# Optimization experiments

Hardware: AMD Instinct MI355X
Metric: run time of the kernel (lower is better)

Reference implementation:

```python
import jax, jax.numpy as jnp
import numpy as np

N_NODES = 50000


def sage_conv(x, src, dst, Wl, bl, Wr, n_nodes):
    # PyG SAGEConv (aggr='mean', root_weight=True, bias on lin_l):
    #   out = lin_l(mean_{j in N(i)} x_j) + lin_r(x_i)
    msg = x[src]  # [E, d] gather
    s = jax.ops.segment_sum(msg, dst, num_segments=n_nodes)  # [N, d]
    cnt = jax.ops.segment_sum(jnp.ones((src.shape[0], 1), x.dtype), dst,
                              num_segments=n_nodes)  # [N, 1]
    agg = s / jnp.maximum(cnt, 1.0)
    return agg @ Wl.T + bl + x @ Wr.T


def setup_inputs() -> dict:
    key = jax.random.key(0)
    ks = jax.random.split(key, 8)
    in_c, hid_c, out_c = 256, 256, 2
    x = jax.random.normal(ks[0], (N_NODES, in_c), dtype=jnp.float32)
    edge_index = jax.random.randint(ks[1], (2, 800000), 0, N_NODES, dtype=jnp.int64)
    def lin(k, fan_out, fan_in):
        bound = 1.0 / np.sqrt(fan_in)
        return jax.random.uniform(k, (fan_out, fan_in), jnp.float32, -bound, bound)
    return {
        "x": x,
        "edge_index": edge_index,
        "W1l": lin(ks[2], hid_c, in_c),
        "b1": jnp.zeros((hid_c,), jnp.float32),
        "W1r": lin(ks[3], hid_c, in_c),
        "W2l": lin(ks[4], out_c, hid_c),
        "b2": jnp.zeros((out_c,), jnp.float32),
        "W2r": lin(ks[5], out_c, hid_c),
    }


def reference(x, edge_index, W1l, b1, W1r, W2l, b2, W2r):
    src, dst = edge_index[0], edge_index[1]
    h = sage_conv(x, src, dst, W1l, b1, W1r, N_NODES)
    h = jax.nn.relu(h)
    # dropout is identity in eval mode (training=False)
    out = sage_conv(h, src, dst, W2l, b2, W2r, N_NODES)
    return jax.nn.log_softmax(out, axis=1)
```

## Files before the change

### kernel.cpp

```cpp
#include <hip/hip_runtime.h>
#include <math.h>

#define DIM 256
#define GBM 128
#define GBN 128
#define GBK 64
#define LDS_K 72
#define SCHUNK 1024

typedef short bf16x8 __attribute__((ext_vector_type(8)));
typedef float f32x4 __attribute__((ext_vector_type(4)));

__device__ __forceinline__ ushort f2bf(float f) {
  uint u = __float_as_uint(f);
  u += 0x7fffu + ((u >> 16) & 1u);
  return (ushort)(u >> 16);
}
__device__ __forceinline__ float bf2f(uint bits) {
  return __uint_as_float(bits << 16);
}

__global__ __launch_bounds__(256) void convert_x(
    const float4* __restrict__ x4, ushort* __restrict__ xb, int n4) {
  int i = blockIdx.x * blockDim.x + threadIdx.x;
  const int stride = gridDim.x * blockDim.x;
  for (; i < n4; i += stride) {
    const float4 v = x4[i];
    ushort4 o;
    o.x = f2bf(v.x); o.y = f2bf(v.y); o.z = f2bf(v.z); o.w = f2bf(v.w);
    *(ushort4*)&xb[i * 4] = o;
  }
}

__global__ __launch_bounds__(256) void wcat_kernel(
    const float* __restrict__ Wl, const float* __restrict__ Wr,
    const float* __restrict__ W2l, const float* __restrict__ W2r,
    ushort* __restrict__ Wb, ushort* __restrict__ W2b) {
  const int idx = blockIdx.x * 256 + threadIdx.x;
  if (idx < 131072) {
    const int n = idx >> 9, k = idx & 511;
    const float v = (k < 256) ? Wl[n * 256 + k] : Wr[n * 256 + (k - 256)];
    Wb[idx] = f2bf(v);
  } else {
    const int w2 = idx - 131072;
    const int row = w2 >> 8, k = w2 & 255;
    float v = 0.f;
    if (row < 2)      v = W2l[row * 256 + k];
    else if (row < 4) v = W2r[(row - 2) * 256 + k];
    W2b[w2] = f2bf(v);
  }
}

__global__ __launch_bounds__(256) void hist_kernel(
    const int* __restrict__ dst, int* __restrict__ deg, int E) {
  int e = blockIdx.x * blockDim.x + threadIdx.x;
  if (e < E) atomicAdd(&deg[dst[e]], 1);
}

__global__ __launch_bounds__(256) void scan_partial(
    const int* __restrict__ deg, int* __restrict__ bsum, int M) {
  const int base = blockIdx.x * SCHUNK + threadIdx.x * 4;
  int s = 0;
  if (base + 3 < M) {
    const int4 v = *(const int4*)(deg + base);
    s = v.x + v.y + v.z + v.w;
  } else {
    for (int j = 0; j < 4; ++j) if (base + j < M) s += deg[base + j];
  }
  #pragma unroll
  for (int off = 32; off; off >>= 1) s += __shfl_xor(s, off);
  __shared__ int ws[4];
  if ((threadIdx.x & 63) == 0) ws[threadIdx.x >> 6] = s;
  __syncthreads();
  if (threadIdx.x == 0) bsum[blockIdx.x] = ws[0] + ws[1] + ws[2] + ws[3];
}

__global__ __launch_bounds__(1024) void scan_sums(
    int* __restrict__ bsum, int nb) {
  __shared__ int sh[1024];
  const int t = threadIdx.x;
  const int orig = (t < nb) ? bsum[t] : 0;
  sh[t] = orig;
  __syncthreads();
  for (int off = 1; off < 1024; off <<= 1) {
    const int v = sh[t];
    const int u = (t >= off) ? sh[t - off] : 0;
    __syncthreads();
    sh[t] = v + u;
    __syncthreads();
  }
  if (t < nb) bsum[t] = sh[t] - orig;
}

__global__ __launch_bounds__(256) void scan_finalize(
    const int* __restrict__ deg, const int* __restrict__ bsum,
    int* __restrict__ rowptr, int* __restrict__ fill,
    float* __restrict__ invc, int M) {
  const int t = threadIdx.x;
  const int lane = t & 63;
  const int wid = t >> 6;
  const int base = blockIdx.x * SCHUNK + t * 4;
  int d[4];
  #pragma unroll
  for (int j = 0; j < 4; ++j) d[j] = (base + j < M) ? deg[base + j] : 0;
  const int tsum = d[0] + d[1] + d[2] + d[3];
  int v = tsum;
  #pragma unroll
  for (int off = 1; off < 64; off <<= 1) {
    const int u = __shfl_up(v, off);
    if (lane >= off) v += u;
  }
  __shared__ int wtot[4];
  if (lane == 63) wtot[wid] = v;
  __syncthreads();
  int wbase = 0;
  for (int w = 0; w < wid; ++w) wbase += wtot[w];
  int run = bsum[blockIdx.x] + wbase + v - tsum;
  #pragma unroll
  for (int j = 0; j < 4; ++j) {
    const int idx = base + j;
    if (idx < M) {
      rowptr[idx] = run;
      fill[idx]   = run;
      invc[idx]   = 1.0f / fmaxf((float)d[j], 1.0f);
      run += d[j];
      if (idx == M - 1) rowptr[M] = run;
    }
  }
}

__global__ __launch_bounds__(256) void scatter_edges(
    const int* __restrict__ src, const int* __restrict__ dst,
    int* __restrict__ fill, int* __restrict__ esrc, int E) {
  int e = blockIdx.x * blockDim.x + threadIdx.x;
  if (e < E) {
    const int pos = atomicAdd(&fill[dst[e]], 1);
    esrc[pos] = src[e];
  }
}

__global__ __launch_bounds__(256) void gather1(
    const ushort* __restrict__ xb, const int* __restrict__ esrc,
    const int* __restrict__ rowptr, const float* __restrict__ invc,
    ushort* __restrict__ aggb, int M) {
  const int lane = threadIdx.x & 63;
  const int wave = threadIdx.x >> 6;
  const int half = lane >> 5;
  const int fl   = lane & 31;
  const int i = blockIdx.x * 4 + wave;
  if (i >= M) return;
  const int k0 = rowptr[i];
  const int k1 = rowptr[i + 1];
  float s0 = 0.f, s1 = 0.f, s2 = 0.f, s3 = 0.f;
  float s4 = 0.f, s5 = 0.f, s6 = 0.f, s7 = 0.f;

#define ACC(v)                                                  \
  do {                                                          \
    s0 += bf2f((v).x & 0xffffu); s1 += bf2f((v).x >> 16);       \
    s2 += bf2f((v).y & 0xffffu); s3 += bf2f((v).y >> 16);       \
    s4 += bf2f((v).z & 0xffffu); s5 += bf2f((v).z >> 16);       \
    s6 += bf2f((v).w & 0xffffu); s7 += bf2f((v).w >> 16);       \
  } while (0)

  int k = k0;
  for (; k + 3 < k1; k += 4) {
    const int e0 = esrc[k + half];
    const int e1 = esrc[k + 2 + half];
    const uint4 v0 = *(const uint4*)(xb + (size_t)e0 * DIM + fl * 8);
    const uint4 v1 = *(const uint4*)(xb + (size_t)e1 * DIM + fl * 8);
    ACC(v0);
    ACC(v1);
  }
  for (; k + 1 < k1; k += 2) {
    const int e = esrc[k + half];
    const uint4 v = *(const uint4*)(xb + (size_t)e * DIM + fl * 8);
    ACC(v);
  }
  if (k < k1 && half == 0) {
    const uint4 v = *(const uint4*)(xb + (size_t)esrc[k] * DIM + fl * 8);
    ACC(v);
  }
#undef ACC

  s0 += __shfl_xor(s0, 32); s1 += __shfl_xor(s1, 32);
  s2 += __shfl_xor(s2, 32); s3 += __shfl_xor(s3, 32);
  s4 += __shfl_xor(s4, 32); s5 += __shfl_xor(s5, 32);
  s6 += __shfl_xor(s6, 32); s7 += __shfl_xor(s7, 32);

  if (half == 0) {
    const float inv = invc[i];
    uint4 o;
    o.x = (uint)f2bf(s0 * inv) | ((uint)f2bf(s1 * inv) << 16);
    o.y = (uint)f2bf(s2 * inv) | ((uint)f2bf(s3 * inv) << 16);
    o.z = (uint)f2bf(s4 * inv) | ((uint)f2bf(s5 * inv) << 16);
    o.w = (uint)f2bf(s6 * inv) | ((uint)f2bf(s7 * inv) << 16);
    *(uint4*)(aggb + (size_t)i * DIM + fl * 8) = o;
  }
}

__global__ __launch_bounds__(256) void gemm1_mfma(
    const ushort* __restrict__ Ab, const ushort* __restrict__ Xb,
    const ushort* __restrict__ Wb, const float* __restrict__ b1,
    ushort* __restrict__ Hb, int M) {
  __shared__ __align__(16) ushort As[GBM * LDS_K];
  __shared__ __align__(16) ushort Bs[GBN * LDS_K];

  const int tid  = threadIdx.x;
  const int lane = tid & 63;
  const int wave = tid >> 6;
  const int wm = wave >> 1, wn = wave & 1;
  const int row0 = blockIdx.x * GBM;
  const int col0 = blockIdx.y * GBN;

  const int lr = tid >> 3;
  const int lc = tid & 7;

  const int frow = lane & 15;
  const int fk   = (lane >> 4) * 8;

  f32x4 acc[4][4] = {};

  for (int kt = 0; kt < 512; kt += GBK) {
    const ushort* srcA = (kt < 256) ? Ab : Xb;
    const int kofs = kt & 255;
    #pragma unroll
    for (int i = 0; i < 4; ++i) {
      const int r = lr + i * 32;
      const int grow = row0 + r;
      uint4 v = make_uint4(0, 0, 0, 0);
      if (grow < M) v = *(const uint4*)(srcA + (size_t)grow * DIM + kofs + lc * 8);
      *(uint4*)&As[r * LDS_K + lc * 8] = v;
    }
    #pragma unroll
    for (int i = 0; i < 4; ++i) {
      const int r = lr + i * 32;
      const uint4 v = *(const uint4*)(Wb + (size_t)(col0 + r) * 512 + kt + lc * 8);
      *(uint4*)&Bs[r * LDS_K + lc * 8] = v;
    }
    __syncthreads();

    #pragma unroll
    for (int s = 0; s < 2; ++s) {
      bf16x8 a[4], b[4];
      #pragma unroll
      for (int i = 0; i < 4; ++i)
        a[i] = *(const bf16x8*)&As[(wm * 64 + i * 16 + frow) * LDS_K + s * 32 + fk];
      #pragma unroll
      for (int j = 0; j < 4; ++j)
        b[j] = *(const bf16x8*)&Bs[(wn * 64 + j * 16 + frow) * LDS_K + s * 32 + fk];
      #pragma unroll
      for (int i = 0; i < 4; ++i)
        #pragma unroll
        for (int j = 0; j < 4; ++j)
          acc[i][j] = __builtin_amdgcn_mfma_f32_16x16x32_bf16(a[i], b[j], acc[i][j], 0, 0, 0);
    }
    __syncthreads();
  }

  #pragma unroll
  for (int i = 0; i < 4; ++i) {
    #pragma unroll
    for (int j = 0; j < 4; ++j) {
      const int col = col0 + wn * 64 + j * 16 + (lane & 15);
      const float bias = b1[col];
      #pragma unroll
      for (int r = 0; r < 4; ++r) {
        const int grow = row0 + wm * 64 + i * 16 + (lane >> 4) * 4 + r;
        if (grow < M) {
          const float v = fmaxf(acc[i][j][r] + bias, 0.f);
          Hb[(size_t)grow * DIM + col] = f2bf(v);
        }
      }
    }
  }
}

__global__ __launch_bounds__(256) void proj2_mfma(
    const ushort* __restrict__ Hb, const ushort* __restrict__ W2b,
    float* __restrict__ Y4v, int M) {
  const int lane = threadIdx.x & 63;
  const int wave = threadIdx.x >> 6;
  const int row0 = (blockIdx.x * 4 + wave) * 16;
  if (row0 >= M) return;
  const int frow = lane & 15;
  const int fk   = (lane >> 4) * 8;

  f32x4 acc = {};
  #pragma unroll
  for (int s = 0; s < 8; ++s) {
    bf16x8 a = {};
    if (row0 + frow < M)
      a = *(const bf16x8*)(Hb + (size_t)(row0 + frow) * DIM + s * 32 + fk);
    const bf16x8 b = *(const bf16x8*)(W2b + frow * DIM + s * 32 + fk);
    acc = __builtin_amdgcn_mfma_f32_16x16x32_bf16(a, b, acc, 0, 0, 0);
  }
  const int col = lane & 15;
  if (col < 4) {
    #pragma unroll
    for (int r = 0; r < 4; ++r) {
      const int row = row0 + (lane >> 4) * 4 + r;
      if (row < M) Y4v[(size_t)row * 4 + col] = acc[r];
    }
  }
}

__global__ __launch_bounds__(256) void layer2_finalize(
    const float2* __restrict__ Y2, const int* __restrict__ esrc,
    const int* __restrict__ rowptr, const float* __restrict__ invc,
    const float* __restrict__ b2, float* __restrict__ out, int M) {
  int i = blockIdx.x * blockDim.x + threadIdx.x;
  if (i < M) {
    const int k0 = rowptr[i];
    const int k1 = rowptr[i + 1];
    float a0 = 0.f, a1 = 0.f;
    for (int k = k0; k < k1; ++k) {
      const float2 y = Y2[2 * (size_t)esrc[k]];
      a0 += y.x; a1 += y.y;
    }
    const float inv = invc[i];
    const float2 yr = Y2[2 * (size_t)i + 1];
    const float o0 = a0 * inv + yr.x + b2[0];
    const float o1 = a1 * inv + yr.y + b2[1];
    const float m = fmaxf(o0, o1);
    const float lse = m + logf(expf(o0 - m) + expf(o1 - m));
    out[2 * i + 0] = o0 - lse;
    out[2 * i + 1] = o1 - lse;
  }
}

extern "C" void kernel_launch(void* const* d_in, const int* in_sizes, int n_in,
                              void* d_out, int out_size, void* d_ws, size_t ws_size,
                              hipStream_t stream) {
  const float* x   = (const float*)d_in[0];
  const int*   ei  = (const int*)d_in[1];
  const float* W1l = (const float*)d_in[2];
  const float* b1  = (const float*)d_in[3];
  const float* W1r = (const float*)d_in[4];
  const float* W2l = (const float*)d_in[5];
  const float* b2  = (const float*)d_in[6];
  const float* W2r = (const float*)d_in[7];

  const int E = in_sizes[1] / 2;
  const int M = in_sizes[0] / DIM;
  const int* src = ei;
  const int* dst = ei + E;

  char* ws = (char*)d_ws;
  size_t off = 0;
  ushort* xb   = (ushort*)(ws + off); off += (size_t)M * DIM * 2;
  ushort* aggb = (ushort*)(ws + off); off += (size_t)M * DIM * 2;
  ushort* Hb   = (ushort*)(ws + off); off += (size_t)M * DIM * 2;
  ushort* Wb   = (ushort*)(ws + off); off += (size_t)256 * 512 * 2;
  ushort* W2b  = (ushort*)(ws + off); off += (size_t)16 * 256 * 2;
  float* Y4v   = (float*)(ws + off);  off += (size_t)M * 4 * 4;
  float* invc  = (float*)(ws + off);  off += (size_t)M * 4;
  int* deg     = (int*)(ws + off);    off += (size_t)M * 4;
  int* fill    = (int*)(ws + off);    off += (size_t)M * 4;
  int* rowptr  = (int*)(ws + off);    off += (size_t)(M + 1) * 4;
  int* bsum    = (int*)(ws + off);    off += 1024 * 4;
  int* esrc    = (int*)(ws + off);    off += (size_t)E * 4;

  hipMemsetAsync(deg, 0, (size_t)M * 4, stream);

  const int EB = (E + 255) / 256;
  const int NB = (M + SCHUNK - 1) / SCHUNK;

  convert_x<<<1024, 256, 0, stream>>>((const float4*)x, xb, M * DIM / 4);
  wcat_kernel<<<528, 256, 0, stream>>>(W1l, W1r, W2l, W2r, Wb, W2b);
  hist_kernel<<<EB, 256, 0, stream>>>(dst, deg, E);
  scan_partial<<<NB, 256, 0, stream>>>(deg, bsum, M);
  scan_sums<<<1, 1024, 0, stream>>>(bsum, NB);
  scan_finalize<<<NB, 256, 0, stream>>>(deg, bsum, rowptr, fill, invc, M);
  scatter_edges<<<EB, 256, 0, stream>>>(src, dst, fill, esrc, E);
  gather1<<<(M + 3) / 4, 256, 0, stream>>>(xb, esrc, rowptr, invc, aggb, M);

  dim3 g1((M + GBM - 1) / GBM, DIM / GBN);
  gemm1_mfma<<<g1, 256, 0, stream>>>(aggb, xb, Wb, b1, Hb, M);

  proj2_mfma<<<(M / 16 + 3) / 4 + 1, 256, 0, stream>>>(Hb, W2b, Y4v, M);
  layer2_finalize<<<(M + 255) / 256, 256, 0, stream>>>(
      (const float2*)Y4v, esrc, rowptr, invc, b2, (float*)d_out, M);
}
```

Baseline: 315.3 us.

## Fuse prep kernels, prefetch GEMM tiles to registers, unroll gathers deeper

Merges the x conversion, weight packing and degree histogram into one grid-stride launch to cut launch overhead. The layer-1 GEMM now loads the next K tile into registers while MFMAs run on the current LDS tile, so global latency overlaps compute. The gather1 edge loop and layer2_finalize are unrolled so more independent row loads are in flight. The cost is higher register pressure in the GEMM and gather, which may reduce occupancy.

```diff
diff --git a/kernel.cpp b/kernel.cpp
--- a/kernel.cpp
+++ b/kernel.cpp
@@ -20,41 +20,33 @@
   return __uint_as_float(bits << 16);
 }
 
-__global__ __launch_bounds__(256) void convert_x(
-    const float4* __restrict__ x4, ushort* __restrict__ xb, int n4) {
-  int i = blockIdx.x * blockDim.x + threadIdx.x;
+__global__ __launch_bounds__(256) void prep_kernel(
+    const float4* __restrict__ x4, ushort* __restrict__ xb, int n4,
+    const float* __restrict__ Wl, const float* __restrict__ Wr,
+    const float* __restrict__ W2l, const float* __restrict__ W2r,
+    ushort* __restrict__ Wb, ushort* __restrict__ W2b,
+    const int* __restrict__ dst, int* __restrict__ deg, int E) {
+  const int t0 = blockIdx.x * blockDim.x + threadIdx.x;
   const int stride = gridDim.x * blockDim.x;
-  for (; i < n4; i += stride) {
+  for (int i = t0; i < n4; i += stride) {
     const float4 v = x4[i];
     ushort4 o;
     o.x = f2bf(v.x); o.y = f2bf(v.y); o.z = f2bf(v.z); o.w = f2bf(v.w);
     *(ushort4*)&xb[i * 4] = o;
   }
-}
-
-__global__ __launch_bounds__(256) void wcat_kernel(
-    const float* __restrict__ Wl, const float* __restrict__ Wr,
-    const float* __restrict__ W2l, const float* __restrict__ W2r,
-    ushort* __restrict__ Wb, ushort* __restrict__ W2b) {
-  const int idx = blockIdx.x * 256 + threadIdx.x;
-  if (idx < 131072) {
-    const int n = idx >> 9, k = idx & 511;
+  if (t0 < 131072) {
+    const int n = t0 >> 9, k = t0 & 511;
     const float v = (k < 256) ? Wl[n * 256 + k] : Wr[n * 256 + (k - 256)];
-    Wb[idx] = f2bf(v);
-  } else {
-    const int w2 = idx - 131072;
+    Wb[t0] = f2bf(v);
+  } else if (t0 < 135168) {
+    const int w2 = t0 - 131072;
     const int row = w2 >> 8, k = w2 & 255;
     float v = 0.f;
     if (row < 2)      v = W2l[row * 256 + k];
     else if (row < 4) v = W2r[(row - 2) * 256 + k];
     W2b[w2] = f2bf(v);
   }
-}
-
-__global__ __launch_bounds__(256) void hist_kernel(
-    const int* __restrict__ dst, int* __restrict__ deg, int E) {
-  int e = blockIdx.x * blockDim.x + threadIdx.x;
-  if (e < E) atomicAdd(&deg[dst[e]], 1);
+  for (int e = t0; e < E; e += stride) atomicAdd(&deg[dst[e]], 1);
 }
 
 __global__ __launch_bounds__(256) void scan_partial(
@@ -163,13 +155,16 @@
   } while (0)
 
   int k = k0;
-  for (; k + 3 < k1; k += 4) {
-    const int e0 = esrc[k + half];
+  for (; k + 7 < k1; k += 8) {
+    const int e0 = esrc[k + 0 + half];
     const int e1 = esrc[k + 2 + half];
+    const int e2 = esrc[k + 4 + half];
+    const int e3 = esrc[k + 6 + half];
     const uint4 v0 = *(const uint4*)(xb + (size_t)e0 * DIM + fl * 8);
     const uint4 v1 = *(const uint4*)(xb + (size_t)e1 * DIM + fl * 8);
-    ACC(v0);
-    ACC(v1);
+    const uint4 v2 = *(const uint4*)(xb + (size_t)e2 * DIM + fl * 8);
+    const uint4 v3 = *(const uint4*)(xb + (size_t)e3 * DIM + fl * 8);
+    ACC(v0); ACC(v1); ACC(v2); ACC(v3);
   }
   for (; k + 1 < k1; k += 2) {
     const int e = esrc[k + half];
@@ -219,26 +214,44 @@
   const int fk   = (lane >> 4) * 8;
 
   f32x4 acc[4][4] = {};
-
-  for (int kt = 0; kt < 512; kt += GBK) {
-    const ushort* srcA = (kt < 256) ? Ab : Xb;
-    const int kofs = kt & 255;
+  uint4 ga[4], gb[4];
+
+#define LOADR(T)                                                               \
+  do {                                                                         \
+    const ushort* srcA = ((T) < 4) ? Ab : Xb;                                  \
+    const int kofs = ((T) * GBK) & 255;                                        \
+    _Pragma("unroll")                                                          \
+    for (int i_ = 0; i_ < 4; ++i_) {                                           \
+      const int r_ = lr + i_ * 32;                                             \
+      const int grow_ = row0 + r_;                                             \
+      ga[i_] = (grow_ < M)                                                     \
+          ? *(const uint4*)(srcA + (size_t)grow_ * DIM + kofs + lc * 8)        \
+          : make_uint4(0, 0, 0, 0);                                            \
+      gb[i_] = *(const uint4*)(Wb + (size_t)(col0 + r_) * 512 + (T) * GBK + lc * 8); \
+    }                                                                          \
+  } while (0)
+
+  LOADR(0);
+  #pragma unroll
+  for (int t = 0; t < 8; ++t) {
     #pragma unroll
     for (int i = 0; i < 4; ++i) {
       const int r = lr + i * 32;
-      const int grow = row0 + r;
-      uint4 v = make_uint4(0, 0, 0, 0);
-      if (grow < M) v = *(const uint4*)(srcA + (size_t)grow * DIM + kofs + lc * 8);
-      *(uint4*)&As[r * LDS_K + lc * 8] = v;
-    }
-    #pragma unroll
-    for (int i = 0; i < 4; ++i) {
-      const int r = lr + i * 32;
-      const uint4 v = *(const uint4*)(Wb + (size_t)(col0 + r) * 512 + kt + lc * 8);
-      *(uint4*)&Bs[r * LDS_K + lc * 8] = v;
+      *(uint4*)&As[r * LDS_K + lc * 8] = ga[i];
+      *(uint4*)&Bs[r * LDS_K + lc * 8] = gb[i];
     }
     __syncthreads();
-
+    if (t < 7) {
+      switch (t + 1) {
+        case 1: LOADR(1); break;
+        case 2: LOADR(2); break;
+        case 3: LOADR(3); break;
+        case 4: LOADR(4); break;
+        case 5: LOADR(5); break;
+        case 6: LOADR(6); break;
+        case 7: LOADR(7); break;
+      }
+    }
     #pragma unroll
     for (int s = 0; s < 2; ++s) {
       bf16x8 a[4], b[4];
@@ -256,6 +269,7 @@
     }
     __syncthreads();
   }
+#undef LOADR
 
   #pragma unroll
   for (int i = 0; i < 4; ++i) {
@@ -313,7 +327,17 @@
     const int k0 = rowptr[i];
     const int k1 = rowptr[i + 1];
     float a0 = 0.f, a1 = 0.f;
-    for (int k = k0; k < k1; ++k) {
+    int k = k0;
+    for (; k + 3 < k1; k += 4) {
+      const int e0 = esrc[k], e1 = esrc[k + 1], e2 = esrc[k + 2], e3 = esrc[k + 3];
+      const float2 y0 = Y2[2 * (size_t)e0];
+      const float2 y1 = Y2[2 * (size_t)e1];
+      const float2 y2 = Y2[2 * (size_t)e2];
+      const float2 y3 = Y2[2 * (size_t)e3];
+      a0 += y0.x + y1.x + y2.x + y3.x;
+      a1 += y0.y + y1.y + y2.y + y3.y;
+    }
+    for (; k < k1; ++k) {
       const float2 y = Y2[2 * (size_t)esrc[k]];
       a0 += y.x; a1 += y.y;
     }
@@ -365,9 +389,8 @@
   const int EB = (E + 255) / 256;
   const int NB = (M + SCHUNK - 1) / SCHUNK;
 
-  convert_x<<<1024, 256, 0, stream>>>((const float4*)x, xb, M * DIM / 4);
-  wcat_kernel<<<528, 256, 0, stream>>>(W1l, W1r, W2l, W2r, Wb, W2b);
-  hist_kernel<<<EB, 256, 0, stream>>>(dst, deg, E);
+  prep_kernel<<<2048, 256, 0, stream>>>((const float4*)x, xb, M * DIM / 4,
+                                        W1l, W1r, W2l, W2r, Wb, W2b, dst, deg, E);
   scan_partial<<<NB, 256, 0, stream>>>(deg, bsum, M);
   scan_sums<<<1, 1024, 0, stream>>>(bsum, NB);
   scan_finalize<<<NB, 256, 0, stream>>>(deg, bsum, rowptr, fill, invc, M);
```

Result: no change. 318.8 us (+1.1%).
